# Kernel optimization log

Hardware: AMD Instinct MI355X
Metric: run time of the kernel (lower is better)

The kernel has to match this reference:

```python
import jax, jax.numpy as jnp
import numpy as np

N, IN, OUT, T = 65536, 256, 256, 8


def setup_inputs() -> dict:
    key = jax.random.key(0)
    k1, k2, k3, k4 = jax.random.split(key, 4)
    x = jax.random.normal(k1, (N, IN), dtype=jnp.float32)
    types = jax.random.randint(k2, (N,), 0, T, dtype=jnp.int32)
    # xavier_uniform for W: limit = sqrt(6 / (fan_in + fan_out)) with fan computed
    # on the last two dims (out_size, in_size)
    limit = float(np.sqrt(6.0 / (IN + OUT)))
    W = jax.random.uniform(k3, (T, OUT, IN), dtype=jnp.float32, minval=-limit, maxval=limit)
    # original inits b to zeros; use small random values so the bias path is exercised
    b = 0.01 * jax.random.normal(k4, (T, OUT), dtype=jnp.float32)
    return {"x": x, "types": types, "W": W, "b": b}


def reference(x, types, W, b):
    # out[i] = W[types[i]] @ x[i] + b[types[i]]
    # Grouped-GEMM expressed as a loop over the small fixed set of types,
    # avoiding the huge [N, OUT, IN] gather of W[types].
    num_types = W.shape[0]
    out = b[types]  # [N, OUT]
    for t in range(num_types):
        mask = (types == t)[:, None]  # [N, 1]
        out = out + jnp.where(mask, x @ W[t].T, jnp.float32(0.0))
    return out
```

## Files before the change

### kernel.cpp

```cpp
#include <hip/hip_runtime.h>
#include <stdint.h>


#define NROWS 65536
#define NTYPES 8
#define KDIM 256
#define ODIM 256
#define BM 32
#define MAX_TILES (NROWS / BM + NTYPES)

typedef __attribute__((ext_vector_type(8))) short short8;
typedef __attribute__((ext_vector_type(4))) float f32x4;

__device__ __forceinline__ unsigned short f2bf(float f) {
    unsigned int u = __float_as_uint(f);
    u += 0x7fffu + ((u >> 16) & 1u);
    return (unsigned short)(u >> 16);
}

__global__ void prep_bucket_kernel(const float* __restrict__ W,
                                   unsigned short* __restrict__ Wp,
                                   const int* __restrict__ types,
                                   int* __restrict__ cnt,
                                   int* __restrict__ idx) {
    const int b = blockIdx.x;
    if (b < 256) {
        const int gid = b * 256 + threadIdx.x;
        const int R   = gid >> 5;
        const int c32 = gid & 31;
        const int t  = R >> 8;
        const int r  = R & 255;
        const int f  = r >> 4;
        const int rr = r & 15;
        const int q  = c32 >> 2;
        const int l  = (c32 & 3) * 16 + rr;
        const float* src = W + (size_t)R * KDIM + c32 * 8;
        const float4 v0 = *(const float4*)src;
        const float4 v1 = *(const float4*)(src + 4);
        ushort4 p0, p1;
        p0.x = f2bf(v0.x); p0.y = f2bf(v0.y); p0.z = f2bf(v0.z); p0.w = f2bf(v0.w);
        p1.x = f2bf(v1.x); p1.y = f2bf(v1.y); p1.z = f2bf(v1.z); p1.w = f2bf(v1.w);
        ushort4* dst = (ushort4*)(Wp + (size_t)(((t * 16 + f) * 8 + q) * 512 + l * 8));
        dst[0] = p0; dst[1] = p1;
    } else {
        __shared__ int h[NTYPES];
        __shared__ int base[NTYPES];
        int i = (b - 256) * 256 + threadIdx.x;
        if (threadIdx.x < NTYPES) h[threadIdx.x] = 0;
        __syncthreads();
        int t = types[i];
        int r = atomicAdd(&h[t], 1);
        __syncthreads();
        if (threadIdx.x < NTYPES)
            base[threadIdx.x] = atomicAdd(&cnt[threadIdx.x], h[threadIdx.x]);
        __syncthreads();
        idx[t * NROWS + base[t] + r] = i;
    }
}

__global__ void plan_kernel(const int* __restrict__ cnt, int2* __restrict__ plan) {
    __shared__ int start[NTYPES + 1];
    if (threadIdx.x == 0) {
        int acc = 0;
        for (int t = 0; t < NTYPES; ++t) {
            start[t] = acc;
            acc += (cnt[t] + BM - 1) / BM;
        }
        start[NTYPES] = acc;
    }
    __syncthreads();
    #pragma unroll
    for (int t = 0; t < NTYPES; ++t) {
        const int s = start[t], e = start[t + 1], c = cnt[t];
        for (int i = s + (int)threadIdx.x; i < e; i += 256)
            plan[i] = make_int2((((i - s) * BM) << 4) | t, c);
    }
    for (int i = start[NTYPES] + (int)threadIdx.x; i < MAX_TILES; i += 256)
        plan[i] = make_int2(-1, 0);
}

__global__ __launch_bounds__(256, 2)
void gemm_kernel(const float* __restrict__ x,
                 const float* __restrict__ bias,
                 const unsigned short* __restrict__ Wp,
                 const int2* __restrict__ plan,
                 const int* __restrict__ idx,
                 float* __restrict__ out) {
    const int2 pe = plan[blockIdx.x];
    if (pe.x < 0) return;
    const int t = pe.x & 15;
    const int m0 = pe.x >> 4;
    const int count = pe.y;

    __shared__ unsigned short As[BM * KDIM];
    __shared__ int idx_s[BM];
    char* AsB = (char*)As;

    const int tid = threadIdx.x;
    const int wave = tid >> 6;
    const int lane = tid & 63;
    const int lr = lane & 15;
    const int lq = lane >> 4;

    const unsigned short* wbase =
        Wp + (size_t)t * (16 * 8 * 512) + (size_t)(wave * 4) * 8 * 512 + lane * 8;
    short8 bf[8][4];
    #pragma unroll
    for (int q = 0; q < 8; ++q)
        #pragma unroll
        for (int j = 0; j < 4; ++j)
            bf[q][j] = *(const short8*)(wbase + j * 4096 + q * 512);
    __builtin_amdgcn_sched_barrier(0);

    float bv[4];
    #pragma unroll
    for (int j = 0; j < 4; ++j)
        bv[j] = bias[t * ODIM + wave * 64 + j * 16 + lr];

    {
        const int srow = tid >> 3;
        const int sc   = tid & 7;
        const int gr = m0 + srow;
        const int xr = idx[t * NROWS + (gr < count ? gr : count - 1)];
        if (sc == 0) idx_s[srow] = xr;
        const float* xs = x + (size_t)xr * KDIM;
        float4 av[8];
        #pragma unroll
        for (int s = 0; s < 8; ++s)
            av[s] = *(const float4*)(xs + (s * 8 + sc) * 4);
        #pragma unroll
        for (int s = 0; s < 8; ++s) {
            const int slot = s * 8 + sc;
            ushort4 pk;
            pk.x = f2bf(av[s].x); pk.y = f2bf(av[s].y);
            pk.z = f2bf(av[s].z); pk.w = f2bf(av[s].w);
            const int c = slot >> 1;
            *(ushort4*)(AsB + srow * 512 + ((c ^ (srow & 7)) * 16) + (slot & 1) * 8) = pk;
        }
    }
    __syncthreads();

    f32x4 acc[2][4] = {};

    #pragma unroll
    for (int q = 0; q < 8; ++q) {
        short8 af[2];
        #pragma unroll
        for (int i = 0; i < 2; ++i) {
            const int row = i * 16 + lr;
            af[i] = *(const short8*)(AsB + row * 512
                                         + (((q << 2) + lq) ^ (row & 7)) * 16);
        }
        #pragma unroll
        for (int i = 0; i < 2; ++i)
            #pragma unroll
            for (int j = 0; j < 4; ++j)
                acc[i][j] = __builtin_amdgcn_mfma_f32_16x16x32_bf16(
                    af[i], bf[q][j], acc[i][j], 0, 0, 0);
    }

    #pragma unroll
    for (int i = 0; i < 2; ++i) {
        #pragma unroll
        for (int r = 0; r < 4; ++r) {
            const int lm = i * 16 + lq * 4 + r;
            const int gr = m0 + lm;
            if (gr < count) {
                const size_t orow = (size_t)idx_s[lm] * ODIM;
                #pragma unroll
                for (int j = 0; j < 4; ++j)
                    out[orow + wave * 64 + j * 16 + lr] = acc[i][j][r] + bv[j];
            }
        }
    }
}

extern "C" void kernel_launch(void* const* d_in, const int* in_sizes, int n_in,
                              void* d_out, int out_size, void* d_ws, size_t ws_size,
                              hipStream_t stream) {
    const float* x     = (const float*)d_in[0];
    const int*   types = (const int*)d_in[1];
    const float* W     = (const float*)d_in[2];
    const float* b     = (const float*)d_in[3];
    float* out = (float*)d_out;

    char* ws = (char*)d_ws;
    int* cnt = (int*)ws;
    int2* plan = (int2*)(ws + 256);
    int* idx = (int*)(ws + 32768);
    unsigned short* Wp = (unsigned short*)(ws + 32768 + (size_t)NTYPES * NROWS * sizeof(int));

    hipMemsetAsync(cnt, 0, NTYPES * sizeof(int), stream);
    prep_bucket_kernel<<<512, 256, 0, stream>>>(W, Wp, types, cnt, idx);
    plan_kernel<<<1, 256, 0, stream>>>(cnt, plan);
    gemm_kernel<<<MAX_TILES, 256, 0, stream>>>(x, b, Wp, plan, idx, out);
}
```

Measured before the change: 141.1 us.

## Give each wave an independent 16-row group and stream W fragments from global

After: 210.6 us. 1.49x slower.

```diff
diff --git a/kernel.cpp b/kernel.cpp
--- a/kernel.cpp
+++ b/kernel.cpp
@@ -6,8 +6,9 @@
 #define NTYPES 8
 #define KDIM 256
 #define ODIM 256
-#define BM 32
-#define MAX_TILES (NROWS / BM + NTYPES)
+#define GM 16
+#define MAX_GROUPS (NROWS / GM + NTYPES)
+#define NBLK ((MAX_GROUPS + 3) / 4)
 
 typedef __attribute__((ext_vector_type(8))) short short8;
 typedef __attribute__((ext_vector_type(4))) float f32x4;
@@ -64,7 +65,7 @@
         int acc = 0;
         for (int t = 0; t < NTYPES; ++t) {
             start[t] = acc;
-            acc += (cnt[t] + BM - 1) / BM;
+            acc += (cnt[t] + GM - 1) / GM;
         }
         start[NTYPES] = acc;
     }
@@ -73,104 +74,75 @@
     for (int t = 0; t < NTYPES; ++t) {
         const int s = start[t], e = start[t + 1], c = cnt[t];
         for (int i = s + (int)threadIdx.x; i < e; i += 256)
-            plan[i] = make_int2((((i - s) * BM) << 4) | t, c);
+            plan[i] = make_int2((((i - s) * GM) << 4) | t, c);
     }
-    for (int i = start[NTYPES] + (int)threadIdx.x; i < MAX_TILES; i += 256)
+    for (int i = start[NTYPES] + (int)threadIdx.x; i < MAX_GROUPS; i += 256)
         plan[i] = make_int2(-1, 0);
 }
 
-__global__ __launch_bounds__(256, 2)
+__global__ __launch_bounds__(256, 4)
 void gemm_kernel(const float* __restrict__ x,
                  const float* __restrict__ bias,
                  const unsigned short* __restrict__ Wp,
                  const int2* __restrict__ plan,
                  const int* __restrict__ idx,
                  float* __restrict__ out) {
-    const int2 pe = plan[blockIdx.x];
+    const int gw = blockIdx.x * 4 + (threadIdx.x >> 6);
+    const int2 pe = plan[gw];
     if (pe.x < 0) return;
     const int t = pe.x & 15;
     const int m0 = pe.x >> 4;
     const int count = pe.y;
 
-    __shared__ unsigned short As[BM * KDIM];
-    __shared__ int idx_s[BM];
-    char* AsB = (char*)As;
-
-    const int tid = threadIdx.x;
-    const int wave = tid >> 6;
-    const int lane = tid & 63;
+    const int lane = threadIdx.x & 63;
     const int lr = lane & 15;
     const int lq = lane >> 4;
 
-    const unsigned short* wbase =
-        Wp + (size_t)t * (16 * 8 * 512) + (size_t)(wave * 4) * 8 * 512 + lane * 8;
-    short8 bf[8][4];
-    #pragma unroll
-    for (int q = 0; q < 8; ++q)
-        #pragma unroll
-        for (int j = 0; j < 4; ++j)
-            bf[q][j] = *(const short8*)(wbase + j * 4096 + q * 512);
-    __builtin_amdgcn_sched_barrier(0);
+    const int gr = m0 + lr;
+    const int xrow = idx[t * NROWS + (gr < count ? gr : count - 1)];
+    const float* xbase = x + (size_t)xrow * KDIM + lq * 8;
 
-    float bv[4];
-    #pragma unroll
-    for (int j = 0; j < 4; ++j)
-        bv[j] = bias[t * ODIM + wave * 64 + j * 16 + lr];
+    const unsigned short* wb = Wp + (size_t)t * (16 * 8 * 512) + lane * 8;
 
-    {
-        const int srow = tid >> 3;
-        const int sc   = tid & 7;
-        const int gr = m0 + srow;
-        const int xr = idx[t * NROWS + (gr < count ? gr : count - 1)];
-        if (sc == 0) idx_s[srow] = xr;
-        const float* xs = x + (size_t)xr * KDIM;
-        float4 av[8];
-        #pragma unroll
-        for (int s = 0; s < 8; ++s)
-            av[s] = *(const float4*)(xs + (s * 8 + sc) * 4);
-        #pragma unroll
-        for (int s = 0; s < 8; ++s) {
-            const int slot = s * 8 + sc;
-            ushort4 pk;
-            pk.x = f2bf(av[s].x); pk.y = f2bf(av[s].y);
-            pk.z = f2bf(av[s].z); pk.w = f2bf(av[s].w);
-            const int c = slot >> 1;
-            *(ushort4*)(AsB + srow * 512 + ((c ^ (srow & 7)) * 16) + (slot & 1) * 8) = pk;
-        }
-    }
-    __syncthreads();
-
-    f32x4 acc[2][4] = {};
+    f32x4 acc[16] = {};
 
     #pragma unroll
     for (int q = 0; q < 8; ++q) {
-        short8 af[2];
+        const float4 a0 = *(const float4*)(xbase + q * 32);
+        const float4 a1 = *(const float4*)(xbase + q * 32 + 4);
+        short8 af;
+        af[0] = (short)f2bf(a0.x); af[1] = (short)f2bf(a0.y);
+        af[2] = (short)f2bf(a0.z); af[3] = (short)f2bf(a0.w);
+        af[4] = (short)f2bf(a1.x); af[5] = (short)f2bf(a1.y);
+        af[6] = (short)f2bf(a1.z); af[7] = (short)f2bf(a1.w);
         #pragma unroll
-        for (int i = 0; i < 2; ++i) {
-            const int row = i * 16 + lr;
-            af[i] = *(const short8*)(AsB + row * 512
-                                         + (((q << 2) + lq) ^ (row & 7)) * 16);
+        for (int h = 0; h < 2; ++h) {
+            short8 bf[8];
+            #pragma unroll
+            for (int j = 0; j < 8; ++j)
+                bf[j] = *(const short8*)(wb + (size_t)(h * 8 + j) * 4096 + q * 512);
+            #pragma unroll
+            for (int j = 0; j < 8; ++j)
+                acc[h * 8 + j] = __builtin_amdgcn_mfma_f32_16x16x32_bf16(
+                    af, bf[j], acc[h * 8 + j], 0, 0, 0);
         }
-        #pragma unroll
-        for (int i = 0; i < 2; ++i)
-            #pragma unroll
-            for (int j = 0; j < 4; ++j)
-                acc[i][j] = __builtin_amdgcn_mfma_f32_16x16x32_bf16(
-                    af[i], bf[q][j], acc[i][j], 0, 0, 0);
     }
 
+    int rowid[4];
+    bool ok[4];
     #pragma unroll
-    for (int i = 0; i < 2; ++i) {
+    for (int r = 0; r < 4; ++r) {
+        const int rr = m0 + lq * 4 + r;
+        ok[r] = rr < count;
+        rowid[r] = idx[t * NROWS + (rr < count ? rr : count - 1)];
+    }
+    #pragma unroll
+    for (int f = 0; f < 16; ++f) {
+        const float bv = bias[t * ODIM + f * 16 + lr];
         #pragma unroll
         for (int r = 0; r < 4; ++r) {
-            const int lm = i * 16 + lq * 4 + r;
-            const int gr = m0 + lm;
-            if (gr < count) {
-                const size_t orow = (size_t)idx_s[lm] * ODIM;
-                #pragma unroll
-                for (int j = 0; j < 4; ++j)
-                    out[orow + wave * 64 + j * 16 + lr] = acc[i][j][r] + bv[j];
-            }
+            if (ok[r])
+                out[(size_t)rowid[r] * ODIM + f * 16 + lr] = acc[f][r] + bv;
         }
     }
 }
@@ -187,11 +159,11 @@
     char* ws = (char*)d_ws;
     int* cnt = (int*)ws;
     int2* plan = (int2*)(ws + 256);
-    int* idx = (int*)(ws + 32768);
-    unsigned short* Wp = (unsigned short*)(ws + 32768 + (size_t)NTYPES * NROWS * sizeof(int));
+    int* idx = (int*)(ws + 65536);
+    unsigned short* Wp = (unsigned short*)(ws + 65536 + (size_t)NTYPES * NROWS * sizeof(int));
 
     hipMemsetAsync(cnt, 0, NTYPES * sizeof(int), stream);
     prep_bucket_kernel<<<512, 256, 0, stream>>>(W, Wp, types, cnt, idx);
     plan_kernel<<<1, 256, 0, stream>>>(cnt, plan);
-    gemm_kernel<<<MAX_TILES, 256, 0, stream>>>(x, b, Wp, plan, idx, out);
+    gemm_kernel<<<NBLK, 256, 0, stream>>>(x, b, Wp, plan, idx, out);
 }
```
